# Optimization experiments

Hardware: AMD Instinct MI355X
Metric: run time of the kernel (lower is better)

The kernel has to match this reference:

```python
import jax, jax.numpy as jnp
import numpy as np

N = 16384
D_IN = 128
D_OUT = 128


def setup_inputs() -> dict:
    key = jax.random.key(0)
    k_adj, k_feat, k_neigh, k_w = jax.random.split(key, 4)
    adj = jax.random.uniform(k_adj, (N, N), dtype=jnp.float32)
    features = jax.random.normal(k_feat, (N, D_IN), dtype=jnp.float32)
    neigh_feats = jax.random.normal(k_neigh, (N, D_IN), dtype=jnp.float32)
    # xavier-uniform-ish init for Linear(2*D_IN -> D_OUT), weight stored [out, in] like torch
    limit = np.sqrt(2.0) * np.sqrt(6.0 / (2 * D_IN + D_OUT))
    W = jax.random.uniform(k_w, (D_OUT, 2 * D_IN), dtype=jnp.float32,
                           minval=-limit, maxval=limit)
    return {"adj": adj, "features": features, "neigh_feats": neigh_feats, "W": W}


def reference(adj, features, neigh_feats, W):
    # len(neigh_feats) == len(features) -> no fill_diagonal_ in the original.
    # neighbor aggregation with degree normalization (degree + 1)
    deg = jnp.sum(adj, axis=1, keepdims=True) + 1.0           # [N, 1]
    neigh_feature = (adj @ neigh_feats) / deg                  # [N, D_IN]
    data = jnp.concatenate([features, neigh_feature], axis=-1)  # [N, 2*D_IN]
    combined = data @ W.T                                      # [N, D_OUT]
    return combined
```

## Files before the change

### kernel.cpp

```cpp
#include <hip/hip_runtime.h>
#include <hip/hip_bf16.h>
#include <stdint.h>

#define NN 16384
#define BM 64
#define KHALF 8192
#define BKA 128
#define BKB 64
#define NG1 (KHALF / BKA)
#define NKT1 (KHALF / BKB)

typedef __attribute__((ext_vector_type(8))) short bf16x8;
typedef __attribute__((ext_vector_type(4))) float f32x4;
typedef __attribute__((ext_vector_type(4))) unsigned short u16x4;
typedef __attribute__((ext_vector_type(8))) unsigned short u16x8;
typedef __attribute__((ext_vector_type(4))) unsigned int u32x4;

__device__ __forceinline__ unsigned short f2bf(float f) {
    uint32_t u = __builtin_bit_cast(uint32_t, f);
    u += 0x7fffu + ((u >> 16) & 1u);
    return (unsigned short)(u >> 16);
}

__global__ __launch_bounds__(256) void prep_transpose(const float* __restrict__ src,
                                                      unsigned short* __restrict__ dstT) {
    __shared__ unsigned short tl[128][66];
    const int t = threadIdx.x;
    const int r0 = blockIdx.x * 64;
#pragma unroll
    for (int i = 0; i < 8; ++i) {
        int idx = i * 256 + t;
        int r = idx >> 5;
        int s = idx & 31;
        f32x4 v = *(const f32x4*)(src + (size_t)(r0 + r) * 128 + s * 4);
#pragma unroll
        for (int j = 0; j < 4; ++j) tl[s * 4 + j][r] = f2bf(v[j]);
    }
    __syncthreads();
    const int c = t >> 1;
    const int half = t & 1;
#pragma unroll
    for (int j = 0; j < 4; ++j) {
        u16x8 p;
#pragma unroll
        for (int e = 0; e < 8; ++e) p[e] = tl[c][half * 32 + j * 8 + e];
        *(u16x8*)(dstT + (size_t)c * NN + r0 + half * 32 + j * 8) = p;
    }
}

#define MFMA16(a, b, c) __builtin_amdgcn_mfma_f32_16x16x32_bf16(a, b, c, 0, 0, 0)

#define BARRIER() do {                                          \
    asm volatile("s_waitcnt lgkmcnt(0)" ::: "memory");          \
    __builtin_amdgcn_s_barrier();                               \
    __builtin_amdgcn_sched_barrier(0);                          \
} while (0)

__global__ __launch_bounds__(256, 2) void sage_partial(
    const float* __restrict__ adj,
    const unsigned short* __restrict__ neighT,
    float* __restrict__ S,
    float* __restrict__ degW)
{
    __shared__ __align__(16) char smem[65536];
    char* aL = smem;
    char* bL = smem + 32768;

    const int t = threadIdx.x;
    const int lane = t & 63;
    const int wv = t >> 6;
    const int mt = wv >> 1;
    const int nt = wv & 1;
    const size_t row0 = (size_t)(blockIdx.x >> 1) * BM;
    const size_t koff = (size_t)(blockIdx.x & 1) * KHALF;

    const int ra0 = t >> 3;
    const int asl = t & 7;
    const float* aG0 = adj + (row0 + ra0) * (size_t)NN + koff + asl * 4;
    const float* aG1 = aG0 + (size_t)32 * NN;

    int awz[8];
#pragma unroll
    for (int i = 0; i < 8; ++i) {
        int row = (i < 4) ? ra0 : (ra0 + 32);
        int j = i & 3;
        awz[i] = row * 256 + ((j * 64 + asl * 8) ^ ((row & 7) << 4));
    }

    const int br0 = t >> 3;
    const int bcs = (t & 7) * 8;
    const unsigned short* bG = neighT + (size_t)br0 * NN + koff + bcs;
    int bwb[4];
#pragma unroll
    for (int i = 0; i < 4; ++i) {
        int br = br0 + 32 * i;
        bwb[i] = (br * 128 + bcs * 2) ^ ((br & 7) << 4);
    }

    f32x4 acc[2][4];
#pragma unroll
    for (int i = 0; i < 2; ++i)
#pragma unroll
        for (int j = 0; j < 4; ++j) acc[i][j] = (f32x4){0.f, 0.f, 0.f, 0.f};

    float dsum[2] = {0.f, 0.f};

    f32x4 arA[8];
    u32x4 br_[4];

#define ISSUE_A(G) do {                                                       \
    _Pragma("unroll")                                                         \
    for (int i = 0; i < 8; ++i) {                                             \
        const float* p = (i < 4 ? aG0 : aG1) + (size_t)(G) * BKA + (i & 3) * 32; \
        arA[i] = __builtin_nontemporal_load((const f32x4*)p);                 \
    }                                                                         \
} while (0)

#define ISSUE_B(KT) do {                                                      \
    _Pragma("unroll")                                                         \
    for (int i = 0; i < 4; ++i)                                               \
        br_[i] = *(const u32x4*)(bG + (size_t)(32 * i) * NN +                 \
                                 (size_t)(KT) * BKB);                         \
} while (0)

#define STAGE_A(DST) do {                                                     \
    _Pragma("unroll")                                                         \
    for (int i = 0; i < 8; ++i) {                                             \
        f32x4 v = arA[i];                                                     \
        dsum[i >> 2] += (v[0] + v[1]) + (v[2] + v[3]);                        \
        u16x4 p; p.x = f2bf(v[0]); p.y = f2bf(v[1]);                          \
        p.z = f2bf(v[2]); p.w = f2bf(v[3]);                                   \
        *(u16x4*)((DST) + awz[i]) = p;                                        \
    }                                                                         \
} while (0)

#define STAGE_B(BUF) do {                                                     \
    char* bW = bL + (BUF) * 16384;                                            \
    _Pragma("unroll")                                                         \
    for (int i = 0; i < 4; ++i)                                               \
        *(u32x4*)(bW + bwb[i]) = br_[i];                                      \
} while (0)

#define COMPUTE(ABASE, SUB, BBUF) do {                                        \
    const char* aB = (ABASE);                                                 \
    const char* bB = bL + (BBUF) * 16384;                                     \
    _Pragma("unroll")                                                         \
    for (int ks = 0; ks < 2; ++ks) {                                          \
        bf16x8 af[2], bfr[4];                                                 \
        _Pragma("unroll")                                                     \
        for (int ms = 0; ms < 2; ++ms) {                                      \
            int r = mt * 32 + ms * 16 + (lane & 15);                          \
            int off = r * 256 + (((SUB) * 128 + ks * 64 + (lane >> 4) * 16)   \
                      ^ ((r & 7) << 4));                                      \
            af[ms] = *(const bf16x8*)(aB + off);                              \
        }                                                                     \
        _Pragma("unroll")                                                     \
        for (int ns = 0; ns < 4; ++ns) {                                      \
            int c = nt * 64 + ns * 16 + (lane & 15);                          \
            int off = c * 128 + ((ks * 64 + (lane >> 4) * 16)                 \
                      ^ ((c & 7) << 4));                                      \
            bfr[ns] = *(const bf16x8*)(bB + off);                             \
        }                                                                     \
        _Pragma("unroll")                                                     \
        for (int ms = 0; ms < 2; ++ms)                                        \
            _Pragma("unroll")                                                 \
            for (int ns = 0; ns < 4; ++ns)                                    \
                acc[ms][ns] = MFMA16(af[ms], bfr[ns], acc[ms][ns]);           \
    }                                                                         \
} while (0)

    ISSUE_B(0);
    ISSUE_A(0);
    STAGE_B(0);
    STAGE_A(aL);
    BARRIER();

    for (int g = 0; g < NG1; ++g) {
        char* aCur = aL + (g & 1) * 16384;
        char* aNxt = aL + ((g & 1) ^ 1) * 16384;
#pragma unroll
        for (int s = 0; s < 2; ++s) {
            const int kt = g * 2 + s;
            if (kt + 1 < NKT1) ISSUE_B(kt + 1);
            if (s == 0 && g + 1 < NG1) ISSUE_A(g + 1);
            COMPUTE(aCur, s, kt & 1);
            if (kt + 1 < NKT1) STAGE_B((kt + 1) & 1);
            if (s == 1 && g + 1 < NG1) STAGE_A(aNxt);
            BARRIER();
        }
    }

    dsum[0] += __shfl_xor(dsum[0], 1, 64);
    dsum[0] += __shfl_xor(dsum[0], 2, 64);
    dsum[0] += __shfl_xor(dsum[0], 4, 64);
    dsum[1] += __shfl_xor(dsum[1], 1, 64);
    dsum[1] += __shfl_xor(dsum[1], 2, 64);
    dsum[1] += __shfl_xor(dsum[1], 4, 64);
    if (asl == 0) {
        atomicAdd(&degW[row0 + ra0], dsum[0]);
        atomicAdd(&degW[row0 + ra0 + 32], dsum[1]);
    }

#pragma unroll
    for (int ms = 0; ms < 2; ++ms)
#pragma unroll
        for (int ns = 0; ns < 4; ++ns)
#pragma unroll
            for (int j = 0; j < 4; ++j) {
                int r = mt * 32 + ms * 16 + (lane >> 4) * 4 + j;
                int c = nt * 64 + ns * 16 + (lane & 15);
                atomicAdd(&S[(row0 + r) * 128 + c], acc[ms][ns][j]);
            }
}

__global__ __launch_bounds__(256) void sage_epilogue(
    const float* __restrict__ feat,
    const float* __restrict__ W,
    const float* __restrict__ degW,
    float* __restrict__ S)
{
    __shared__ __align__(16) char smem[33024];
    char* dL = smem;
    float* degp = (float*)(smem + 32768);

    const int t = threadIdx.x;
    const int lane = t & 63;
    const int wv = t >> 6;
    const int mt = wv >> 1;
    const int nt = wv & 1;
    const size_t row0 = (size_t)blockIdx.x * BM;

    if (t < 64) degp[t] = degW[row0 + t];

#pragma unroll
    for (int i = 0; i < 8; ++i) {
        int idx = i * 256 + t;
        int r = idx >> 5;
        int s = idx & 31;
        f32x4 v = *(const f32x4*)(feat + (row0 + r) * 128 + s * 4);
        u16x4 p; p.x = f2bf(v[0]); p.y = f2bf(v[1]); p.z = f2bf(v[2]); p.w = f2bf(v[3]);
        int off = (r * 512 + s * 8) ^ ((r & 7) << 4);
        *(u16x4*)(dL + off) = p;
    }
    __syncthreads();

#pragma unroll
    for (int i = 0; i < 8; ++i) {
        int idx = i * 256 + t;
        int r = idx >> 5;
        int s = idx & 31;
        f32x4 v = *(const f32x4*)(S + (row0 + r) * 128 + s * 4);
        float inv = 1.0f / (degp[r] + 1.0f);
        u16x4 p; p.x = f2bf(v[0] * inv); p.y = f2bf(v[1] * inv);
        p.z = f2bf(v[2] * inv); p.w = f2bf(v[3] * inv);
        int off = (r * 512 + 256 + s * 8) ^ ((r & 7) << 4);
        *(u16x4*)(dL + off) = p;
    }
    __syncthreads();

    f32x4 acc2[2][4];
#pragma unroll
    for (int i = 0; i < 2; ++i)
#pragma unroll
        for (int j = 0; j < 4; ++j) acc2[i][j] = (f32x4){0.f, 0.f, 0.f, 0.f};

#pragma unroll
    for (int ks = 0; ks < 8; ++ks) {
        bf16x8 af[2], bfr[4];
#pragma unroll
        for (int ms = 0; ms < 2; ++ms) {
            int r = mt * 32 + ms * 16 + (lane & 15);
            int off = r * 512 + ((ks * 64 + (lane >> 4) * 16) ^ ((r & 7) << 4));
            af[ms] = *(const bf16x8*)(dL + off);
        }
#pragma unroll
        for (int ns = 0; ns < 4; ++ns) {
            int c = nt * 64 + ns * 16 + (lane & 15);
            int k0 = ks * 32 + (lane >> 4) * 8;
            f32x4 w0 = *(const f32x4*)(W + (size_t)c * 256 + k0);
            f32x4 w1 = *(const f32x4*)(W + (size_t)c * 256 + k0 + 4);
            u16x8 p;
            p[0] = f2bf(w0[0]); p[1] = f2bf(w0[1]); p[2] = f2bf(w0[2]); p[3] = f2bf(w0[3]);
            p[4] = f2bf(w1[0]); p[5] = f2bf(w1[1]); p[6] = f2bf(w1[2]); p[7] = f2bf(w1[3]);
            bfr[ns] = __builtin_bit_cast(bf16x8, p);
        }
#pragma unroll
        for (int ms = 0; ms < 2; ++ms)
#pragma unroll
            for (int ns = 0; ns < 4; ++ns)
                acc2[ms][ns] = MFMA16(af[ms], bfr[ns], acc2[ms][ns]);
    }

#pragma unroll
    for (int ms = 0; ms < 2; ++ms)
#pragma unroll
        for (int ns = 0; ns < 4; ++ns)
#pragma unroll
            for (int j = 0; j < 4; ++j) {
                int r = mt * 32 + ms * 16 + (lane >> 4) * 4 + j;
                int c = nt * 64 + ns * 16 + (lane & 15);
                S[(row0 + r) * 128 + c] = acc2[ms][ns][j];
            }
}

extern "C" void kernel_launch(void* const* d_in, const int* in_sizes, int n_in,
                              void* d_out, int out_size, void* d_ws, size_t ws_size,
                              hipStream_t stream) {
    const float* adj = (const float*)d_in[0];
    const float* feat = (const float*)d_in[1];
    const float* neigh = (const float*)d_in[2];
    const float* W = (const float*)d_in[3];
    float* S = (float*)d_out;
    unsigned short* neighT = (unsigned short*)d_ws;
    float* degW = (float*)((char*)d_ws + (size_t)4 * 1024 * 1024);

    hipMemsetAsync(d_out, 0, (size_t)NN * 128 * sizeof(float), stream);
    hipMemsetAsync(degW, 0, (size_t)NN * sizeof(float), stream);
    prep_transpose<<<NN / 64, 256, 0, stream>>>(neigh, neighT);
    sage_partial<<<(NN / BM) * 2, 256, 0, stream>>>(adj, neighT, S, degW);
    sage_epilogue<<<NN / BM, 256, 0, stream>>>(feat, W, degW, S);
}
```

Baseline: 233.1 us.

## Pre-tile neighbor features into MFMA fragment layout and load B directly to registers

The transpose prep kernel now writes the bf16 neighbor features in a tiled layout that matches the MFMA B-fragment order. The main kernel loads B fragments straight from global memory into registers, double-buffered, and no longer stages them through LDS. This halves shared memory use and removes one barrier per k-subtile, which may improve occupancy and cut LDS traffic. The cost is more live registers and more global or L2 reads, since each wave now loads its own B fragments instead of sharing them through LDS.

```diff
diff --git a/kernel.cpp b/kernel.cpp
--- a/kernel.cpp
+++ b/kernel.cpp
@@ -39,12 +39,14 @@
     __syncthreads();
     const int c = t >> 1;
     const int half = t & 1;
+    const int ktile = (r0 >> 5) + half;
 #pragma unroll
     for (int j = 0; j < 4; ++j) {
         u16x8 p;
 #pragma unroll
         for (int e = 0; e < 8; ++e) p[e] = tl[c][half * 32 + j * 8 + e];
-        *(u16x8*)(dstT + (size_t)c * NN + r0 + half * 32 + j * 8) = p;
+        size_t dst = ((size_t)ktile * 8 + (c >> 4)) * 512 + (c & 15) * 32 + j * 8;
+        *(u16x8*)(dstT + dst) = p;
     }
 }
 
@@ -62,9 +64,8 @@
     float* __restrict__ S,
     float* __restrict__ degW)
 {
-    __shared__ __align__(16) char smem[65536];
+    __shared__ __align__(16) char smem[32768];
     char* aL = smem;
-    char* bL = smem + 32768;
 
     const int t = threadIdx.x;
     const int lane = t & 63;
@@ -87,15 +88,8 @@
         awz[i] = row * 256 + ((j * 64 + asl * 8) ^ ((row & 7) << 4));
     }
 
-    const int br0 = t >> 3;
-    const int bcs = (t & 7) * 8;
-    const unsigned short* bG = neighT + (size_t)br0 * NN + koff + bcs;
-    int bwb[4];
-#pragma unroll
-    for (int i = 0; i < 4; ++i) {
-        int br = br0 + 32 * i;
-        bwb[i] = (br * 128 + bcs * 2) ^ ((br & 7) << 4);
-    }
+    const unsigned short* bT = neighT + ((koff >> 5) * 8 + nt * 4) * 512
+                               + (lane & 15) * 32 + (lane >> 4) * 8;
 
     f32x4 acc[2][4];
 #pragma unroll
@@ -106,7 +100,7 @@
     float dsum[2] = {0.f, 0.f};
 
     f32x4 arA[8];
-    u32x4 br_[4];
+    u32x4 brF[8], brG[8];
 
 #define ISSUE_A(G) do {                                                       \
     _Pragma("unroll")                                                         \
@@ -116,11 +110,13 @@
     }                                                                         \
 } while (0)
 
-#define ISSUE_B(KT) do {                                                      \
+#define ISSUE_B(BR, KT) do {                                                  \
     _Pragma("unroll")                                                         \
-    for (int i = 0; i < 4; ++i)                                               \
-        br_[i] = *(const u32x4*)(bG + (size_t)(32 * i) * NN +                 \
-                                 (size_t)(KT) * BKB);                         \
+    for (int ns = 0; ns < 4; ++ns)                                            \
+        _Pragma("unroll")                                                     \
+        for (int ks = 0; ks < 2; ++ks)                                        \
+            BR[ns * 2 + ks] = *(const u32x4*)(bT +                            \
+                ((size_t)((KT) * 2 + ks) * 8 + ns) * 512);                    \
 } while (0)
 
 #define STAGE_A(DST) do {                                                     \
@@ -134,19 +130,11 @@
     }                                                                         \
 } while (0)
 
-#define STAGE_B(BUF) do {                                                     \
-    char* bW = bL + (BUF) * 16384;                                            \
-    _Pragma("unroll")                                                         \
-    for (int i = 0; i < 4; ++i)                                               \
-        *(u32x4*)(bW + bwb[i]) = br_[i];                                      \
-} while (0)
-
-#define COMPUTE(ABASE, SUB, BBUF) do {                                        \
+#define COMPUTE(ABASE, SUB, BR) do {                                          \
     const char* aB = (ABASE);                                                 \
-    const char* bB = bL + (BBUF) * 16384;                                     \
     _Pragma("unroll")                                                         \
     for (int ks = 0; ks < 2; ++ks) {                                          \
-        bf16x8 af[2], bfr[4];                                                 \
+        bf16x8 af[2];                                                         \
         _Pragma("unroll")                                                     \
         for (int ms = 0; ms < 2; ++ms) {                                      \
             int r = mt * 32 + ms * 16 + (lane & 15);                          \
@@ -155,39 +143,31 @@
             af[ms] = *(const bf16x8*)(aB + off);                              \
         }                                                                     \
         _Pragma("unroll")                                                     \
-        for (int ns = 0; ns < 4; ++ns) {                                      \
-            int c = nt * 64 + ns * 16 + (lane & 15);                          \
-            int off = c * 128 + ((ks * 64 + (lane >> 4) * 16)                 \
-                      ^ ((c & 7) << 4));                                      \
-            bfr[ns] = *(const bf16x8*)(bB + off);                             \
-        }                                                                     \
-        _Pragma("unroll")                                                     \
         for (int ms = 0; ms < 2; ++ms)                                        \
             _Pragma("unroll")                                                 \
             for (int ns = 0; ns < 4; ++ns)                                    \
-                acc[ms][ns] = MFMA16(af[ms], bfr[ns], acc[ms][ns]);           \
+                acc[ms][ns] = MFMA16(af[ms],                                  \
+                    __builtin_bit_cast(bf16x8, BR[ns * 2 + ks]),              \
+                    acc[ms][ns]);                                             \
     }                                                                         \
 } while (0)
 
-    ISSUE_B(0);
+    ISSUE_B(brF, 0);
     ISSUE_A(0);
-    STAGE_B(0);
     STAGE_A(aL);
     BARRIER();
 
     for (int g = 0; g < NG1; ++g) {
         char* aCur = aL + (g & 1) * 16384;
         char* aNxt = aL + ((g & 1) ^ 1) * 16384;
-#pragma unroll
-        for (int s = 0; s < 2; ++s) {
-            const int kt = g * 2 + s;
-            if (kt + 1 < NKT1) ISSUE_B(kt + 1);
-            if (s == 0 && g + 1 < NG1) ISSUE_A(g + 1);
-            COMPUTE(aCur, s, kt & 1);
-            if (kt + 1 < NKT1) STAGE_B((kt + 1) & 1);
-            if (s == 1 && g + 1 < NG1) STAGE_A(aNxt);
-            BARRIER();
-        }
+        const bool more = (g + 1 < NG1);
+        ISSUE_B(brG, 2 * g + 1);
+        if (more) ISSUE_A(g + 1);
+        COMPUTE(aCur, 0, brF);
+        if (more) ISSUE_B(brF, 2 * g + 2);
+        COMPUTE(aCur, 1, brG);
+        if (more) STAGE_A(aNxt);
+        BARRIER();
     }
 
     dsum[0] += __shfl_xor(dsum[0], 1, 64);
```

Measured after the change: 289.6 us. 1.24x slower.
